# Optimization experiments

Measured on AMD Instinct MI355X. Metric: run time of the kernel, lower is better.

Reference implementation:

```python
import jax, jax.numpy as jnp
import numpy as np

B, J = 131072, 24
# SMPL skeleton parent indices (root = joint 0)
SMPL_PARENTS = np.array([-1, 0, 0, 0, 1, 2, 3, 4, 5, 6, 7, 8, 9, 9, 9, 12, 13, 14, 16, 17, 18, 19, 20, 21], dtype=np.int64)


def setup_inputs() -> dict:
    key = jax.random.key(0)
    k1, k2 = jax.random.split(key)
    positions = jax.random.normal(k1, (B, J, 3), dtype=jnp.float32)
    rotations = jax.random.normal(k2, (B, J, 4), dtype=jnp.float32)
    return {"parents": SMPL_PARENTS, "positions": positions, "rotations": rotations}


def _quat_to_rotmat(q):
    # q: [B, J, 4] (w, x, y, z); normalize then standard unit-quaternion rotation matrix
    q = q / jnp.linalg.norm(q, axis=-1, keepdims=True)
    qw, qx, qy, qz = q[..., 0], q[..., 1], q[..., 2], q[..., 3]
    x2, y2, z2 = qx + qx, qy + qy, qz + qz
    xx, yy, zz = qx * x2, qy * y2, qz * z2
    xy, yz, xz = qx * y2, qy * z2, qx * z2
    wx, wy, wz = qw * x2, qw * y2, qw * z2
    row0 = jnp.stack([1.0 - (yy + zz), xy - wz, xz + wy], axis=-1)
    row1 = jnp.stack([xy + wz, 1.0 - (xx + zz), yz - wx], axis=-1)
    row2 = jnp.stack([xz - wy, yz + wx, 1.0 - (xx + yy)], axis=-1)
    return jnp.stack([row0, row1, row2], axis=-2)  # [B, J, 3, 3]


def _local_transforms(positions, rotations):
    R = _quat_to_rotmat(rotations)                       # [B, J, 3, 3]
    top = jnp.concatenate([R, positions[..., None]], axis=-1)  # [B, J, 3, 4]
    bottom = jnp.broadcast_to(
        jnp.array([0.0, 0.0, 0.0, 1.0], dtype=rotations.dtype), top.shape[:2] + (1, 4))
    return jnp.concatenate([top, bottom], axis=-2)       # [B, J, 4, 4]


def reference(parents, positions, rotations):
    parents = np.asarray(parents)  # static skeleton topology
    locals_ = _local_transforms(positions, rotations)    # [B, J, 4, 4]
    n_joints = parents.shape[0]
    # Sequential parent-child chain over the (small, static) joint tree.
    g = [locals_[:, 0]]
    for jt in range(1, n_joints):
        g.append(jnp.matmul(g[int(parents[jt])], locals_[:, jt]))
    globals_ = jnp.stack(g, axis=1)                      # [B, J, 4, 4]
    p = globals_[:, :, :, 3]                             # homogeneous positions [B, J, 4]
    return p[:, :, :3] / p[:, :, 3:4]                    # [B, J, 3]
```

## Files before the change

kernel.cpp:

```cpp
#include <hip/hip_runtime.h>


typedef float f32x4 __attribute__((ext_vector_type(4)));

struct M { float r0,r1,r2,r3,r4,r5,r6,r7,r8,tx,ty,tz; };

__device__ __forceinline__ M loc(float a, float b, float c, float d,
                                 float px, float py, float pz) {
    float inv = rsqrtf(a*a + b*b + c*c + d*d);
    float qw = a*inv, qx = b*inv, qy = c*inv, qz = d*inv;
    float x2 = qx+qx, y2 = qy+qy, z2 = qz+qz;
    float xx = qx*x2, yy = qy*y2, zz = qz*z2;
    float xy = qx*y2, yz = qy*z2, xz = qx*z2;
    float wx = qw*x2, wy = qw*y2, wz = qw*z2;
    M m;
    m.r0 = 1.f-(yy+zz); m.r1 = xy-wz;       m.r2 = xz+wy;
    m.r3 = xy+wz;       m.r4 = 1.f-(xx+zz); m.r5 = yz-wx;
    m.r6 = xz-wy;       m.r7 = yz+wx;       m.r8 = 1.f-(xx+yy);
    m.tx = px; m.ty = py; m.tz = pz;
    return m;
}

__device__ __forceinline__ M mul(const M& a, const M& b) {
    M c;
    c.r0 = a.r0*b.r0 + a.r1*b.r3 + a.r2*b.r6;
    c.r1 = a.r0*b.r1 + a.r1*b.r4 + a.r2*b.r7;
    c.r2 = a.r0*b.r2 + a.r1*b.r5 + a.r2*b.r8;
    c.r3 = a.r3*b.r0 + a.r4*b.r3 + a.r5*b.r6;
    c.r4 = a.r3*b.r1 + a.r4*b.r4 + a.r5*b.r7;
    c.r5 = a.r3*b.r2 + a.r4*b.r5 + a.r5*b.r8;
    c.r6 = a.r6*b.r0 + a.r7*b.r3 + a.r8*b.r6;
    c.r7 = a.r6*b.r1 + a.r7*b.r4 + a.r8*b.r7;
    c.r8 = a.r6*b.r2 + a.r7*b.r5 + a.r8*b.r8;
    c.tx = a.r0*b.tx + a.r1*b.ty + a.r2*b.tz + a.tx;
    c.ty = a.r3*b.tx + a.r4*b.ty + a.r5*b.tz + a.ty;
    c.tz = a.r6*b.tx + a.r7*b.ty + a.r8*b.tz + a.tz;
    return c;
}

#define SPB    64
#define RPITCH 97
#define PPITCH 73

constexpr int MT0[6]  = {0,1,2,4,7,10};
constexpr int PR0[6]  = {-1,0,0,1,3,4};
constexpr int MT1[8]  = {0,2,5,8,11,3,6,9};
constexpr int PR1[8]  = {-1,0,1,2,3,0,5,6};
constexpr int MT2[11] = {0,3,6,9,12,15,13,16,18,20,22};
constexpr int PR2[11] = {-1,0,1,2,3,4,3,6,7,8,9};
constexpr int MT3[9]  = {0,3,6,9,14,17,19,21,23};
constexpr int PR3[9]  = {-1,0,1,2,3,4,5,6,7};

template<int NM>
__device__ __forceinline__ void read_pos(const int (&MT)[NM],
                                         const float* __restrict__ P,
                                         float* __restrict__ pb) {
#pragma unroll
    for (int k = 0; k < NM; ++k) {
        pb[3*k+0] = P[3*MT[k]+0];
        pb[3*k+1] = P[3*MT[k]+1];
        pb[3*k+2] = P[3*MT[k]+2];
    }
}

template<int NM>
__device__ __forceinline__ void run_chain(const int (&MT)[NM], const int (&PR)[NM],
                                          int WS,
                                          const float* __restrict__ R,
                                          const float* __restrict__ pb,
                                          float* __restrict__ O) {
    M G[NM];
    G[0] = loc(R[0], R[1], R[2], R[3], pb[0], pb[1], pb[2]);
    if (WS == 0) { O[0]=G[0].tx; O[1]=G[0].ty; O[2]=G[0].tz; }
#pragma unroll
    for (int k = 1; k < NM; ++k) {
        const int j = MT[k];
        M L = loc(R[4*j], R[4*j+1], R[4*j+2], R[4*j+3],
                  pb[3*k], pb[3*k+1], pb[3*k+2]);
        G[k] = mul(G[PR[k]], L);
        if (k >= WS) { O[3*j]=G[k].tx; O[3*j+1]=G[k].ty; O[3*j+2]=G[k].tz; }
    }
}

__global__ __launch_bounds__(256, 3) void fk_kernel(
    const float* __restrict__ rot,
    const float* __restrict__ pos,
    float*       __restrict__ out,
    int B)
{
    __shared__ float ldsR[SPB * RPITCH];
    __shared__ float ldsP[SPB * PPITCH];

    const int t = threadIdx.x;
    const size_t baseR = (size_t)blockIdx.x * (SPB*96);
    const size_t baseP = (size_t)blockIdx.x * (SPB*72);
    const size_t limR  = (size_t)B * 96;
    const size_t limP  = (size_t)B * 72;

    f32x4 vr[6], vp[5];
#pragma unroll
    for (int i = 0; i < 6; ++i) {
        const size_t gi = baseR + (size_t)(i*1024 + 4*t);
        f32x4 v = {0.f,0.f,0.f,0.f};
        if (gi < limR) v = *(const f32x4*)(rot + gi);
        vr[i] = v;
    }
#pragma unroll
    for (int i = 0; i < 5; ++i) {
        const size_t gi = baseP + (size_t)(i*1024 + 4*t);
        f32x4 v = {0.f,0.f,0.f,0.f};
        if ((i < 4 || t < 128) && gi < limP) v = *(const f32x4*)(pos + gi);
        vp[i] = v;
    }
#pragma unroll
    for (int i = 0; i < 6; ++i) {
        const int f = i*1024 + 4*t;
        const int s = f / 96, r = f - 96*s;
        float* d = ldsR + s*RPITCH + r;
        d[0]=vr[i].x; d[1]=vr[i].y; d[2]=vr[i].z; d[3]=vr[i].w;
    }
#pragma unroll
    for (int i = 0; i < 5; ++i) {
        if (i < 4 || t < 128) {
            const int f = i*1024 + 4*t;
            const int s = f / 72, r = f - 72*s;
            float* d = ldsP + s*PPITCH + r;
            d[0]=vp[i].x; d[1]=vp[i].y; d[2]=vp[i].z; d[3]=vp[i].w;
        }
    }
    __syncthreads();

    const int w = t >> 6, l = t & 63;
    const int b = blockIdx.x * SPB + l;
    const bool act = (b < B);
    const float* R = ldsR + l * RPITCH;
    const float* P = ldsP + l * PPITCH;
    float*       O = ldsP + l * PPITCH;

    float pb[33];
    if (act) {
        switch (w) {
            case 0:  read_pos(MT0, P, pb); break;
            case 1:  read_pos(MT1, P, pb); break;
            case 2:  read_pos(MT2, P, pb); break;
            default: read_pos(MT3, P, pb); break;
        }
    }
    __syncthreads();

    if (act) {
        switch (w) {
            case 0:  run_chain(MT0, PR0, 0, R, pb, O); break;
            case 1:  run_chain(MT1, PR1, 2, R, pb, O); break;
            case 2:  run_chain(MT2, PR2, 4, R, pb, O); break;
            default: run_chain(MT3, PR3, 4, R, pb, O); break;
        }
    }
    __syncthreads();

#pragma unroll
    for (int n = 0; n < 5; ++n) {
        if (n < 4 || t < 128) {
            const int F = n*1024 + 4*t;
            const int s = F / 72, r = F - 72*s;
            const size_t gi = baseP + (size_t)F;
            if (gi < limP) {
                f32x4 v = { ldsP[s*PPITCH+r+0], ldsP[s*PPITCH+r+1],
                            ldsP[s*PPITCH+r+2], ldsP[s*PPITCH+r+3] };
                *(f32x4*)(out + gi) = v;
            }
        }
    }
}

extern "C" void kernel_launch(void* const* d_in, const int* in_sizes, int n_in,
                              void* d_out, int out_size, void* d_ws, size_t ws_size,
                              hipStream_t stream) {
    const int B = out_size / 72;
    const void* rot = nullptr;
    const void* pos = nullptr;
    for (int i = 0; i < n_in; ++i) {
        if      (in_sizes[i] == B * 96) rot = d_in[i];
        else if (in_sizes[i] == B * 72) pos = d_in[i];
    }
    if (!rot) rot = d_in[2];
    if (!pos) pos = d_in[1];

    const int grid = (B + SPB - 1) / SPB;
    fk_kernel<<<grid, 256, 0, stream>>>(
        (const float*)rot, (const float*)pos, (float*)d_out, B);
}
```

Baseline: 128.6 us.

## Split joint tree into eight linear chains across eight waves per sample

Moves from four waves per sample-group, each walking a branched subtree, to eight waves that each compute a linear root-to-leaf chain. Each wave recomputes the shared prefix (root to spine) and writes only the joints it owns, chosen with a bitmask. Keeping a single running transform instead of an array of transforms cuts register pressure, and the block grows to 512 threads to improve latency hiding. The cost is extra redundant matrix multiplies along the shared spine.

```diff
diff --git a/kernel.cpp b/kernel.cpp
--- a/kernel.cpp
+++ b/kernel.cpp
@@ -39,17 +39,18 @@
 }
 
 #define SPB    64
+#define NTHR   512
 #define RPITCH 97
 #define PPITCH 73
 
-constexpr int MT0[6]  = {0,1,2,4,7,10};
-constexpr int PR0[6]  = {-1,0,0,1,3,4};
-constexpr int MT1[8]  = {0,2,5,8,11,3,6,9};
-constexpr int PR1[8]  = {-1,0,1,2,3,0,5,6};
-constexpr int MT2[11] = {0,3,6,9,12,15,13,16,18,20,22};
-constexpr int PR2[11] = {-1,0,1,2,3,4,3,6,7,8,9};
-constexpr int MT3[9]  = {0,3,6,9,14,17,19,21,23};
-constexpr int PR3[9]  = {-1,0,1,2,3,4,5,6,7};
+constexpr int MT0[5] = {0,1,4,7,10};
+constexpr int MT1[5] = {0,2,5,8,11};
+constexpr int MT2[6] = {0,3,6,9,12,15};
+constexpr int MT3[6] = {0,3,6,9,13,16};
+constexpr int MT4[8] = {0,3,6,9,13,16,18,20};
+constexpr int MT5[9] = {0,3,6,9,13,16,18,20,22};
+constexpr int MT6[8] = {0,3,6,9,14,17,19,21};
+constexpr int MT7[9] = {0,3,6,9,14,17,19,21,23};
 
 template<int NM>
 __device__ __forceinline__ void read_pos(const int (&MT)[NM],
@@ -64,25 +65,23 @@
 }
 
 template<int NM>
-__device__ __forceinline__ void run_chain(const int (&MT)[NM], const int (&PR)[NM],
-                                          int WS,
+__device__ __forceinline__ void run_chain(const int (&MT)[NM], unsigned wm,
                                           const float* __restrict__ R,
                                           const float* __restrict__ pb,
                                           float* __restrict__ O) {
-    M G[NM];
-    G[0] = loc(R[0], R[1], R[2], R[3], pb[0], pb[1], pb[2]);
-    if (WS == 0) { O[0]=G[0].tx; O[1]=G[0].ty; O[2]=G[0].tz; }
+    M G = loc(R[0], R[1], R[2], R[3], pb[0], pb[1], pb[2]);
+    if (wm & 1u) { O[0]=G.tx; O[1]=G.ty; O[2]=G.tz; }
 #pragma unroll
     for (int k = 1; k < NM; ++k) {
         const int j = MT[k];
         M L = loc(R[4*j], R[4*j+1], R[4*j+2], R[4*j+3],
                   pb[3*k], pb[3*k+1], pb[3*k+2]);
-        G[k] = mul(G[PR[k]], L);
-        if (k >= WS) { O[3*j]=G[k].tx; O[3*j+1]=G[k].ty; O[3*j+2]=G[k].tz; }
+        G = mul(G, L);
+        if ((wm >> k) & 1u) { O[3*j]=G.tx; O[3*j+1]=G.ty; O[3*j+2]=G.tz; }
     }
 }
 
-__global__ __launch_bounds__(256, 3) void fk_kernel(
+__global__ __launch_bounds__(NTHR, 6) void fk_kernel(
     const float* __restrict__ rot,
     const float* __restrict__ pos,
     float*       __restrict__ out,
@@ -97,32 +96,32 @@
     const size_t limR  = (size_t)B * 96;
     const size_t limP  = (size_t)B * 72;
 
-    f32x4 vr[6], vp[5];
+    f32x4 vr[3], vp[3];
 #pragma unroll
-    for (int i = 0; i < 6; ++i) {
-        const size_t gi = baseR + (size_t)(i*1024 + 4*t);
+    for (int i = 0; i < 3; ++i) {
+        const size_t gi = baseR + (size_t)(i*2048 + 4*t);
         f32x4 v = {0.f,0.f,0.f,0.f};
         if (gi < limR) v = *(const f32x4*)(rot + gi);
         vr[i] = v;
     }
 #pragma unroll
-    for (int i = 0; i < 5; ++i) {
-        const size_t gi = baseP + (size_t)(i*1024 + 4*t);
+    for (int i = 0; i < 3; ++i) {
+        const size_t gi = baseP + (size_t)(i*2048 + 4*t);
         f32x4 v = {0.f,0.f,0.f,0.f};
-        if ((i < 4 || t < 128) && gi < limP) v = *(const f32x4*)(pos + gi);
+        if ((i < 2 || t < 128) && gi < limP) v = *(const f32x4*)(pos + gi);
         vp[i] = v;
     }
 #pragma unroll
-    for (int i = 0; i < 6; ++i) {
-        const int f = i*1024 + 4*t;
+    for (int i = 0; i < 3; ++i) {
+        const int f = i*2048 + 4*t;
         const int s = f / 96, r = f - 96*s;
         float* d = ldsR + s*RPITCH + r;
         d[0]=vr[i].x; d[1]=vr[i].y; d[2]=vr[i].z; d[3]=vr[i].w;
     }
 #pragma unroll
-    for (int i = 0; i < 5; ++i) {
-        if (i < 4 || t < 128) {
-            const int f = i*1024 + 4*t;
+    for (int i = 0; i < 3; ++i) {
+        if (i < 2 || t < 128) {
+            const int f = i*2048 + 4*t;
             const int s = f / 72, r = f - 72*s;
             float* d = ldsP + s*PPITCH + r;
             d[0]=vp[i].x; d[1]=vp[i].y; d[2]=vp[i].z; d[3]=vp[i].w;
@@ -137,31 +136,39 @@
     const float* P = ldsP + l * PPITCH;
     float*       O = ldsP + l * PPITCH;
 
-    float pb[33];
+    float pb[27];
     if (act) {
         switch (w) {
-            case 0:  read_pos(MT0, P, pb); break;
-            case 1:  read_pos(MT1, P, pb); break;
-            case 2:  read_pos(MT2, P, pb); break;
-            default: read_pos(MT3, P, pb); break;
+            case 0: read_pos(MT0, P, pb); break;
+            case 1: read_pos(MT1, P, pb); break;
+            case 2: read_pos(MT2, P, pb); break;
+            case 3: read_pos(MT3, P, pb); break;
+            case 4: read_pos(MT4, P, pb); break;
+            case 5: read_pos(MT5, P, pb); break;
+            case 6: read_pos(MT6, P, pb); break;
+            default:read_pos(MT7, P, pb); break;
         }
     }
     __syncthreads();
 
     if (act) {
         switch (w) {
-            case 0:  run_chain(MT0, PR0, 0, R, pb, O); break;
-            case 1:  run_chain(MT1, PR1, 2, R, pb, O); break;
-            case 2:  run_chain(MT2, PR2, 4, R, pb, O); break;
-            default: run_chain(MT3, PR3, 4, R, pb, O); break;
+            case 0: run_chain(MT0, 0b11111u,     R, pb, O); break;
+            case 1: run_chain(MT1, 0b11110u,     R, pb, O); break;
+            case 2: run_chain(MT2, 0b110010u,    R, pb, O); break;
+            case 3: run_chain(MT3, 0b110100u,    R, pb, O); break;
+            case 4: run_chain(MT4, 0b11001000u,  R, pb, O); break;
+            case 5: run_chain(MT5, 0b100000000u, R, pb, O); break;
+            case 6: run_chain(MT6, 0b11110000u,  R, pb, O); break;
+            default:run_chain(MT7, 0b100000000u, R, pb, O); break;
         }
     }
     __syncthreads();
 
 #pragma unroll
-    for (int n = 0; n < 5; ++n) {
-        if (n < 4 || t < 128) {
-            const int F = n*1024 + 4*t;
+    for (int n = 0; n < 3; ++n) {
+        if (n < 2 || t < 128) {
+            const int F = n*2048 + 4*t;
             const int s = F / 72, r = F - 72*s;
             const size_t gi = baseP + (size_t)F;
             if (gi < limP) {
@@ -187,6 +194,6 @@
     if (!pos) pos = d_in[1];
 
     const int grid = (B + SPB - 1) / SPB;
-    fk_kernel<<<grid, 256, 0, stream>>>(
+    fk_kernel<<<grid, NTHR, 0, stream>>>(
         (const float*)rot, (const float*)pos, (float*)d_out, B);
 }
```

Result: slower. 236.8 us (+84.2%).
